# Performance work log

Measured on AMD Instinct MI355X. Metric: run time of the kernel, lower is better.

The kernel has to match this reference:

```python
import jax, jax.numpy as jnp
import numpy as np

N_NODES = 100000
N_EDGES = 625000
D = 128


def setup_inputs() -> dict:
    key = jax.random.key(0)
    ks = jax.random.split(key, 6)
    x = jax.random.normal(ks[0], (N_NODES, D), dtype=jnp.float32)
    src = jax.random.randint(ks[1], (N_EDGES,), 0, N_NODES, dtype=jnp.int32)
    dst = jnp.sort(jax.random.randint(ks[2], (N_EDGES,), 0, N_NODES, dtype=jnp.int32))
    edge_w = jax.random.uniform(ks[3], (N_EDGES,), dtype=jnp.float32)
    # linear layer params (fan-in scaled)
    W = jax.random.normal(ks[4], (D, D), dtype=jnp.float32) / np.sqrt(D)
    b = jnp.zeros((D,), dtype=jnp.float32)
    # highway gate params (glorot-uniform-ish range as in source)
    init_range = np.sqrt(2.0 / (D + D)).astype(np.float32)
    kernel_gate = jax.random.uniform(ks[5], (D, D), dtype=jnp.float32,
                                     minval=-init_range, maxval=init_range)
    bias_gate = jnp.zeros((D,), dtype=jnp.float32)
    return {"x": x, "src": src, "dst": dst, "edge_w": edge_w,
            "W": W, "b": b, "kernel_gate": kernel_gate, "bias_gate": bias_gate}


def reference(x, src, dst, edge_w, W, b, kernel_gate, bias_gate):
    # hidden = Linear(x); dropout is identity in eval mode
    hidden = x @ W.T + b                                  # [N, D]
    # support = spmm(adj, hidden): gather src rows, weight, scatter-add to dst
    msgs = edge_w[:, None] * hidden[src]                  # [E, D]
    support = jax.ops.segment_sum(msgs, dst, num_segments=x.shape[0])
    support = jax.nn.relu(support)                        # act
    # highway gate
    gate = jax.nn.sigmoid(x @ kernel_gate + bias_gate)    # [N, D]
    out = gate * support + (1.0 - gate) * x
    return out
```

## Files before the change

### kernel.cpp

```cpp
#include <hip/hip_runtime.h>

#define DD 128

typedef __attribute__((ext_vector_type(8))) short bf16x8;
typedef __attribute__((ext_vector_type(4))) float f32x4;

__device__ __forceinline__ unsigned int cvt_pk_bf16(float lo, float hi) {
  unsigned int r;
  asm("v_cvt_pk_bf16_f32 %0, %1, %2" : "=v"(r) : "v"(lo), "v"(hi));
  return r;
}
__device__ __forceinline__ float bf_lo(unsigned int v) { return __uint_as_float(v << 16); }
__device__ __forceinline__ float bf_hi(unsigned int v) { return __uint_as_float(v & 0xFFFF0000u); }

__global__ __launch_bounds__(256) void prep_kernel(
    const float* __restrict__ x, const int* __restrict__ dst,
    const float* __restrict__ W, const float* __restrict__ KG,
    unsigned char* __restrict__ xq, float* __restrict__ sx,
    int* __restrict__ row_start, unsigned short* __restrict__ B,
    int N, int E, int ABLK, int BBLK) {
  int blk = blockIdx.x;
  int t = threadIdx.x;
  if (blk < ABLK) {
    int n = blk * 16 + (t >> 4);
    int lr = t & 15;
    if (n < N) {
      const float4* xr = (const float4*)(x + (size_t)n * DD);
      float4 va = xr[lr * 2], vb = xr[lr * 2 + 1];
      float m = fmaxf(fmaxf(fmaxf(fabsf(va.x), fabsf(va.y)), fmaxf(fabsf(va.z), fabsf(va.w))),
                      fmaxf(fmaxf(fabsf(vb.x), fabsf(vb.y)), fmaxf(fabsf(vb.z), fabsf(vb.w))));
#pragma unroll
      for (int d = 1; d < 16; d <<= 1) m = fmaxf(m, __shfl_xor(m, d, 16));
      m = fmaxf(m, 1e-20f);
      float inv = 127.0f / m;
      unsigned int q0 = (unsigned int)(__float2int_rn(va.x * inv) + 128);
      unsigned int q1 = (unsigned int)(__float2int_rn(va.y * inv) + 128);
      unsigned int q2 = (unsigned int)(__float2int_rn(va.z * inv) + 128);
      unsigned int q3 = (unsigned int)(__float2int_rn(va.w * inv) + 128);
      unsigned int q4 = (unsigned int)(__float2int_rn(vb.x * inv) + 128);
      unsigned int q5 = (unsigned int)(__float2int_rn(vb.y * inv) + 128);
      unsigned int q6 = (unsigned int)(__float2int_rn(vb.z * inv) + 128);
      unsigned int q7 = (unsigned int)(__float2int_rn(vb.w * inv) + 128);
      uint2 qp;
      qp.x = q0 | (q1 << 8) | (q2 << 16) | (q3 << 24);
      qp.y = q4 | (q5 << 8) | (q6 << 16) | (q7 << 24);
      ((uint2*)xq)[(size_t)n * 16 + lr] = qp;
      if (lr == 0) sx[n] = m * (1.0f / 127.0f);
    }
  } else if (blk < ABLK + BBLK) {
    int e = (blk - ABLK) * 256 + t;
    if (e <= E) {
      if (e == 0) {
        int d0 = dst[0];
        for (int n = 0; n <= d0; ++n) row_start[n] = 0;
      } else if (e == E) {
        for (int n = dst[E - 1] + 1; n <= N; ++n) row_start[n] = E;
      } else {
        int d = dst[e], dp = dst[e - 1];
        for (int n = dp + 1; n <= d; ++n) row_start[n] = e;
      }
    }
  } else {
    int e2 = (blk - ABLK - BBLK) * 256 + t;
    if (e2 < 2 * DD * DD) {
      int j = e2 >> 7, k = e2 & 127;
      float v = (j < DD) ? W[j * DD + k] : KG[k * DD + (j - DD)];
      B[e2] = (unsigned short)cvt_pk_bf16(v, v);
    }
  }
}

__global__ __launch_bounds__(256, 8) void scatter_agg(
    const unsigned char* __restrict__ xq, const float* __restrict__ sx,
    const int* __restrict__ src, const float* __restrict__ ew,
    const int* __restrict__ row_start, unsigned short* __restrict__ aggb,
    float* __restrict__ sumw, int N, int E) {
  int t = threadIdx.x;
  int wid = t >> 6, lane = t & 63;
  int g = lane >> 4, lr = lane & 15;
  int n = blockIdx.x * 16 + wid * 4 + g;
  bool valid = (n < N);
  int b = valid ? row_start[n] : 0;
  int cnt = valid ? (row_start[n + 1] - b) : 0;
  const uint2* x8 = (const uint2*)xq;

  float a[8];
#pragma unroll
  for (int k = 0; k < 8; ++k) a[k] = 0.f;
  float wsum = 0.f, wsc = 0.f;
  int clampj = cnt > 0 ? cnt - 1 : 0;

  int i = 0;
  while (__any(i < cnt)) {
#pragma unroll
    for (int u = 0; u < 4; ++u) {
      int ii = i + u;
      int jj = ii < clampj ? ii : clampj;
      int j = b + jj;
      if (j > E - 1) j = E - 1;
      float wt = (ii < cnt) ? ew[j] : 0.f;
      int s = src[j];
      float ws = wt * sx[s];
      uint2 v = x8[(size_t)s * 16 + lr];
      wsum += wt;
      wsc += ws;
      a[0] += ws * (float)(v.x & 0xFF);
      a[1] += ws * (float)((v.x >> 8) & 0xFF);
      a[2] += ws * (float)((v.x >> 16) & 0xFF);
      a[3] += ws * (float)(v.x >> 24);
      a[4] += ws * (float)(v.y & 0xFF);
      a[5] += ws * (float)((v.y >> 8) & 0xFF);
      a[6] += ws * (float)((v.y >> 16) & 0xFF);
      a[7] += ws * (float)(v.y >> 24);
    }
    i += 4;
  }
  float c = 128.0f * wsc;
#pragma unroll
  for (int k = 0; k < 8; ++k) a[k] -= c;

  if (valid) {
    uint4 o;
    o.x = cvt_pk_bf16(a[0], a[1]);
    o.y = cvt_pk_bf16(a[2], a[3]);
    o.z = cvt_pk_bf16(a[4], a[5]);
    o.w = cvt_pk_bf16(a[6], a[7]);
    ((uint4*)aggb)[(size_t)n * 16 + lr] = o;
    if (lr == 0) sumw[n] = wsum;
  }
}

__global__ __launch_bounds__(256, 3) void fused_gemm(
    const unsigned char* __restrict__ xq, const float* __restrict__ sx,
    const unsigned short* __restrict__ aggb, const unsigned short* __restrict__ B,
    const float* __restrict__ sumw, const float* __restrict__ bias,
    const float* __restrict__ bg, float* __restrict__ out, int N) {
  __shared__ char smem[32 * 1024];
  unsigned short* sX = (unsigned short*)smem;
  unsigned short* sA = (unsigned short*)(smem + 16384);
  int t = threadIdx.x;
  int wid = t >> 6, lane = t & 63;
  int lr = lane & 15, lk2 = lane >> 4;
  int jw = wid * 32;
  int M0 = blockIdx.x * 64;

  bf16x8 wS[4][2], wG[4][2];
#pragma unroll
  for (int kc = 0; kc < 4; ++kc)
#pragma unroll
    for (int m = 0; m < 2; ++m) {
      int j = jw + m * 16 + lr;
      wS[kc][m] = *(const bf16x8*)(B + (size_t)j * DD + kc * 32 + lk2 * 8);
      wG[kc][m] = *(const bf16x8*)(B + (size_t)(DD + j) * DD + kc * 32 + lk2 * 8);
    }

#pragma unroll
  for (int i = 0; i < 2; ++i) {
    int idx = i * 256 + t;
    int r = idx >> 3;
    int c = idx & 7;
    uint4 v;
    float s;
    if (M0 + r < N) {
      v = ((const uint4*)(xq + (size_t)(M0 + r) * DD))[c];
      s = sx[M0 + r];
    } else {
      v = make_uint4(0, 0, 0, 0);
      s = 0.f;
    }
    float nb = -128.0f * s;
    unsigned int w[4] = {v.x, v.y, v.z, v.w};
    unsigned int o[8];
#pragma unroll
    for (int q = 0; q < 4; ++q) {
      float e0 = fmaf(s, (float)(w[q] & 0xFF), nb);
      float e1 = fmaf(s, (float)((w[q] >> 8) & 0xFF), nb);
      float e2 = fmaf(s, (float)((w[q] >> 16) & 0xFF), nb);
      float e3 = fmaf(s, (float)(w[q] >> 24), nb);
      o[q * 2]     = cvt_pk_bf16(e0, e1);
      o[q * 2 + 1] = cvt_pk_bf16(e2, e3);
    }
    int base = r * 256 + c * 32;
    uint4 lo = {o[0], o[1], o[2], o[3]};
    uint4 hi = {o[4], o[5], o[6], o[7]};
    *(uint4*)((char*)sX + ((base) ^ ((r & 7) << 4)))      = lo;
    *(uint4*)((char*)sX + ((base + 16) ^ ((r & 7) << 4))) = hi;
  }
#pragma unroll
  for (int i = 0; i < 4; ++i) {
    int idx = i * 256 + t;
    int r = idx >> 4, c = idx & 15;
    uint4 va;
    if (M0 + r < N) va = ((const uint4*)(aggb + (size_t)(M0 + r) * DD))[c];
    else            va = make_uint4(0, 0, 0, 0);
    int off = (r * 256 + c * 16) ^ ((r & 7) << 4);
    *(uint4*)((char*)sA + off) = va;
  }
  __syncthreads();

  f32x4 accS[2][4], accG[2][4];
#pragma unroll
  for (int m = 0; m < 2; ++m)
#pragma unroll
    for (int nr = 0; nr < 4; ++nr) {
      accS[m][nr] = (f32x4){0.f, 0.f, 0.f, 0.f};
      accG[m][nr] = (f32x4){0.f, 0.f, 0.f, 0.f};
    }

#pragma unroll
  for (int kc = 0; kc < 4; ++kc) {
    int kb = (kc * 32 + lk2 * 8) * 2;
    bf16x8 af[4], xf[4];
#pragma unroll
    for (int nr = 0; nr < 4; ++nr) {
      int r = nr * 16 + lr;
      int off = (r * 256 + kb) ^ ((r & 7) << 4);
      af[nr] = *(const bf16x8*)((const char*)sA + off);
      xf[nr] = *(const bf16x8*)((const char*)sX + off);
    }
#pragma unroll
    for (int m = 0; m < 2; ++m)
#pragma unroll
      for (int nr = 0; nr < 4; ++nr) {
        accS[m][nr] = __builtin_amdgcn_mfma_f32_16x16x32_bf16(wS[kc][m], af[nr], accS[m][nr], 0, 0, 0);
        accG[m][nr] = __builtin_amdgcn_mfma_f32_16x16x32_bf16(wG[kc][m], xf[nr], accG[m][nr], 0, 0, 0);
      }
  }

  float ba[2][4], bga[2][4];
#pragma unroll
  for (int m = 0; m < 2; ++m) {
    int j0 = jw + m * 16 + lk2 * 4;
    *(float4*)ba[m]  = *(const float4*)&bias[j0];
    *(float4*)bga[m] = *(const float4*)&bg[j0];
  }
#pragma unroll
  for (int nr = 0; nr < 4; ++nr) {
    int node = M0 + nr * 16 + lr;
    if (node < N) {
      float sw = sumw[node];
      int r = nr * 16 + lr;
#pragma unroll
      for (int m = 0; m < 2; ++m) {
        int j0 = jw + m * 16 + lk2 * 4;
        uint2 qx = *(const uint2*)((const char*)sX + ((r * 256 + j0 * 2) ^ ((r & 7) << 4)));
        float xr[4] = {bf_lo(qx.x), bf_hi(qx.x), bf_lo(qx.y), bf_hi(qx.y)};
        f32x4 vs = accS[m][nr], vg = accG[m][nr];
        f32x4 o;
#pragma unroll
        for (int reg = 0; reg < 4; ++reg) {
          float s = fmaxf(vs[reg] + sw * ba[m][reg], 0.f);
          float g = 1.0f / (1.0f + __expf(-(vg[reg] + bga[m][reg])));
          o[reg] = g * s + (1.0f - g) * xr[reg];
        }
        __builtin_nontemporal_store(o, (f32x4*)&out[(size_t)node * DD + j0]);
      }
    }
  }
}

extern "C" void kernel_launch(void* const* d_in, const int* in_sizes, int n_in,
                              void* d_out, int out_size, void* d_ws, size_t ws_size,
                              hipStream_t stream) {
  const float* x   = (const float*)d_in[0];
  const int*   src = (const int*)d_in[1];
  const int*   dst = (const int*)d_in[2];
  const float* ew  = (const float*)d_in[3];
  const float* W   = (const float*)d_in[4];
  const float* b   = (const float*)d_in[5];
  const float* KG  = (const float*)d_in[6];
  const float* bg  = (const float*)d_in[7];
  float* out = (float*)d_out;

  int N = in_sizes[0] / DD;
  int E = in_sizes[1];

  unsigned short* aggb = (unsigned short*)d_ws;
  unsigned char* xq = (unsigned char*)(aggb + (size_t)N * DD);
  float* sx = (float*)(xq + (size_t)N * DD);
  float* sumw = sx + N;
  unsigned short* B = (unsigned short*)(sumw + N);
  int* row_start = (int*)(B + 2 * DD * DD);

  int ABLK = (N + 15) / 16;
  int BBLK = (E + 1 + 255) / 256;
  int CBLK = (2 * DD * DD + 255) / 256;
  prep_kernel<<<ABLK + BBLK + CBLK, 256, 0, stream>>>(x, dst, W, KG, xq, sx,
                                                      row_start, B, N, E, ABLK, BBLK);
  scatter_agg<<<(N + 15) / 16, 256, 0, stream>>>(xq, sx, src, ew, row_start, aggb, sumw, N, E);
  fused_gemm<<<(N + 63) / 64, 256, 0, stream>>>(xq, sx, aggb, B, sumw, b, bg, out, N);
}
```

Before: 73.33 us.

## Split quantized features into column slices and aggregate each slice separately

The int8 node-feature table is stored as four column slices of 32 bytes per node, and the gather-aggregate runs as four launches, one per slice. Each launch's random gathers touch only a 3.2 MB slice, which is meant to stay resident in L2/MALL and cut DRAM traffic from random row reads. The cost is re-reading the src, edge-weight and row_start arrays four times, three extra kernel launches, and narrower 4-byte gathers per lane. The GEMM kernel's loads are updated to read the sliced layout.

```diff
diff --git a/kernel.cpp b/kernel.cpp
--- a/kernel.cpp
+++ b/kernel.cpp
@@ -16,7 +16,7 @@
 __global__ __launch_bounds__(256) void prep_kernel(
     const float* __restrict__ x, const int* __restrict__ dst,
     const float* __restrict__ W, const float* __restrict__ KG,
-    unsigned char* __restrict__ xq, float* __restrict__ sx,
+    unsigned char* __restrict__ xq4, float* __restrict__ sx,
     int* __restrict__ row_start, unsigned short* __restrict__ B,
     int N, int E, int ABLK, int BBLK) {
   int blk = blockIdx.x;
@@ -44,7 +44,8 @@
       uint2 qp;
       qp.x = q0 | (q1 << 8) | (q2 << 16) | (q3 << 24);
       qp.y = q4 | (q5 << 8) | (q6 << 16) | (q7 << 24);
-      ((uint2*)xq)[(size_t)n * 16 + lr] = qp;
+      unsigned char* slice = xq4 + (size_t)(lr >> 2) * N * 32;
+      ((uint2*)(slice + (size_t)n * 32))[lr & 3] = qp;
       if (lr == 0) sx[n] = m * (1.0f / 127.0f);
     }
   } else if (blk < ABLK + BBLK) {
@@ -70,23 +71,21 @@
   }
 }
 
-__global__ __launch_bounds__(256, 8) void scatter_agg(
-    const unsigned char* __restrict__ xq, const float* __restrict__ sx,
+__global__ __launch_bounds__(256, 8) void scatter_agg_q(
+    const unsigned char* __restrict__ xq4, const float* __restrict__ sx,
     const int* __restrict__ src, const float* __restrict__ ew,
     const int* __restrict__ row_start, unsigned short* __restrict__ aggb,
-    float* __restrict__ sumw, int N, int E) {
+    float* __restrict__ sumw, int N, int E, int qq) {
   int t = threadIdx.x;
   int wid = t >> 6, lane = t & 63;
-  int g = lane >> 4, lr = lane & 15;
-  int n = blockIdx.x * 16 + wid * 4 + g;
+  int g = lane >> 3, lr = lane & 7;
+  int n = blockIdx.x * 32 + wid * 8 + g;
   bool valid = (n < N);
   int b = valid ? row_start[n] : 0;
   int cnt = valid ? (row_start[n + 1] - b) : 0;
-  const uint2* x8 = (const uint2*)xq;
-
-  float a[8];
-#pragma unroll
-  for (int k = 0; k < 8; ++k) a[k] = 0.f;
+  const unsigned int* xs = (const unsigned int*)(xq4 + (size_t)qq * N * 32);
+
+  float a[4] = {0.f, 0.f, 0.f, 0.f};
   float wsum = 0.f, wsc = 0.f;
   int clampj = cnt > 0 ? cnt - 1 : 0;
 
@@ -101,37 +100,31 @@
       float wt = (ii < cnt) ? ew[j] : 0.f;
       int s = src[j];
       float ws = wt * sx[s];
-      uint2 v = x8[(size_t)s * 16 + lr];
+      unsigned int v = xs[(size_t)s * 8 + lr];
       wsum += wt;
       wsc += ws;
-      a[0] += ws * (float)(v.x & 0xFF);
-      a[1] += ws * (float)((v.x >> 8) & 0xFF);
-      a[2] += ws * (float)((v.x >> 16) & 0xFF);
-      a[3] += ws * (float)(v.x >> 24);
-      a[4] += ws * (float)(v.y & 0xFF);
-      a[5] += ws * (float)((v.y >> 8) & 0xFF);
-      a[6] += ws * (float)((v.y >> 16) & 0xFF);
-      a[7] += ws * (float)(v.y >> 24);
+      a[0] += ws * (float)(v & 0xFF);
+      a[1] += ws * (float)((v >> 8) & 0xFF);
+      a[2] += ws * (float)((v >> 16) & 0xFF);
+      a[3] += ws * (float)(v >> 24);
     }
     i += 4;
   }
   float c = 128.0f * wsc;
 #pragma unroll
-  for (int k = 0; k < 8; ++k) a[k] -= c;
+  for (int k = 0; k < 4; ++k) a[k] -= c;
 
   if (valid) {
-    uint4 o;
+    uint2 o;
     o.x = cvt_pk_bf16(a[0], a[1]);
     o.y = cvt_pk_bf16(a[2], a[3]);
-    o.z = cvt_pk_bf16(a[4], a[5]);
-    o.w = cvt_pk_bf16(a[6], a[7]);
-    ((uint4*)aggb)[(size_t)n * 16 + lr] = o;
-    if (lr == 0) sumw[n] = wsum;
+    *(uint2*)&aggb[(size_t)n * DD + qq * 32 + lr * 4] = o;
+    if (lr == 0 && qq == 0) sumw[n] = wsum;
   }
 }
 
 __global__ __launch_bounds__(256, 3) void fused_gemm(
-    const unsigned char* __restrict__ xq, const float* __restrict__ sx,
+    const unsigned char* __restrict__ xq4, const float* __restrict__ sx,
     const unsigned short* __restrict__ aggb, const unsigned short* __restrict__ B,
     const float* __restrict__ sumw, const float* __restrict__ bias,
     const float* __restrict__ bg, float* __restrict__ out, int N) {
@@ -162,7 +155,7 @@
     uint4 v;
     float s;
     if (M0 + r < N) {
-      v = ((const uint4*)(xq + (size_t)(M0 + r) * DD))[c];
+      v = *(const uint4*)(xq4 + ((size_t)(c >> 1) * N + (M0 + r)) * 32 + (c & 1) * 16);
       s = sx[M0 + r];
     } else {
       v = make_uint4(0, 0, 0, 0);
@@ -276,8 +269,8 @@
   int E = in_sizes[1];
 
   unsigned short* aggb = (unsigned short*)d_ws;
-  unsigned char* xq = (unsigned char*)(aggb + (size_t)N * DD);
-  float* sx = (float*)(xq + (size_t)N * DD);
+  unsigned char* xq4 = (unsigned char*)(aggb + (size_t)N * DD);
+  float* sx = (float*)(xq4 + (size_t)N * DD);
   float* sumw = sx + N;
   unsigned short* B = (unsigned short*)(sumw + N);
   int* row_start = (int*)(B + 2 * DD * DD);
@@ -285,8 +278,10 @@
   int ABLK = (N + 15) / 16;
   int BBLK = (E + 1 + 255) / 256;
   int CBLK = (2 * DD * DD + 255) / 256;
-  prep_kernel<<<ABLK + BBLK + CBLK, 256, 0, stream>>>(x, dst, W, KG, xq, sx,
+  prep_kernel<<<ABLK + BBLK + CBLK, 256, 0, stream>>>(x, dst, W, KG, xq4, sx,
                                                       row_start, B, N, E, ABLK, BBLK);
-  scatter_agg<<<(N + 15) / 16, 256, 0, stream>>>(xq, sx, src, ew, row_start, aggb, sumw, N, E);
-  fused_gemm<<<(N + 63) / 64, 256, 0, stream>>>(xq, sx, aggb, B, sumw, b, bg, out, N);
-}
+  int SBLK = (N + 31) / 32;
+  for (int qq = 0; qq < 4; ++qq)
+    scatter_agg_q<<<SBLK, 256, 0, stream>>>(xq4, sx, src, ew, row_start, aggb, sumw, N, E, qq);
+  fused_gemm<<<(N + 63) / 64, 256, 0, stream>>>(xq4, sx, aggb, B, sumw, b, bg, out, N);
+}
```

New measurement: 120.1 us. 1.64x slower.
